# Kernel optimization log

Hardware: AMD Instinct MI355X
Metric: run time of the kernel (lower is better)

Reference implementation:

```python
import jax, jax.numpy as jnp
import numpy as np

DN = ('NCHW', 'OIHW', 'NCHW')

def conv(x, w, b, stride=1, pad=0):
    y = jax.lax.conv_general_dilated(x, w, (stride, stride), ((pad, pad), (pad, pad)), dimension_numbers=DN)
    return y + b[None, :, None, None]

def maxpool(x, k, s):
    return jax.lax.reduce_window(x, -jnp.inf, jax.lax.max, (1, 1, k, k), (1, 1, s, s), 'VALID')

def bilinear_resize(x, oh, ow):
    # torch F.interpolate(mode='bilinear', align_corners=False)
    H, W = x.shape[2], x.shape[3]
    def grid(n_in, n_out):
        c = (jnp.arange(n_out, dtype=x.dtype) + 0.5) * (n_in / n_out) - 0.5
        c = jnp.clip(c, 0.0, n_in - 1)
        lo = jnp.floor(c).astype(jnp.int32)
        hi = jnp.minimum(lo + 1, n_in - 1)
        return lo, hi, c - lo
    r0, r1, wr = grid(H, oh)
    c0, c1, wc = grid(W, ow)
    top = x[:, :, r0, :] * (1 - wr)[None, None, :, None] + x[:, :, r1, :] * wr[None, None, :, None]
    return top[:, :, :, c0] * (1 - wc) + top[:, :, :, c1] * wc

def setup_inputs():
    key = jax.random.key(0)
    ks = jax.random.split(key, 18)
    s = 0.02
    d = {}
    d['x'] = jax.random.normal(ks[0], (16, 3, 448, 448), jnp.float32)
    d['w1'] = jax.random.normal(ks[1], (64, 3, 7, 7), jnp.float32) * s
    d['b1'] = jax.random.normal(ks[2], (64,), jnp.float32) * s
    d['w3'] = jax.random.normal(ks[3], (192, 64, 3, 3), jnp.float32) * s
    d['b3'] = jax.random.normal(ks[4], (192,), jnp.float32) * s
    d['w4'] = jax.random.normal(ks[5], (256, 192, 3, 3), jnp.float32) * s
    d['b4'] = jax.random.normal(ks[6], (256,), jnp.float32) * s
    d['w7'] = jax.random.normal(ks[7], (512, 256, 2, 2), jnp.float32) * s
    d['b7'] = jax.random.normal(ks[8], (512,), jnp.float32) * s
    d['w8'] = jax.random.normal(ks[9], (1024, 512, 2, 2), jnp.float32) * s
    d['b8'] = jax.random.normal(ks[10], (1024,), jnp.float32) * s
    d['wu'] = jax.random.normal(ks[11], (1024, 1024, 2, 2), jnp.float32) * s
    d['bu'] = jax.random.normal(ks[12], (1024,), jnp.float32) * s
    d['lc_w'] = jax.random.normal(ks[13], (1024, 256, 7, 7, 3, 3), jnp.float32) * s
    d['lc_b'] = jax.random.normal(ks[14], (256, 7, 7), jnp.float32) * s
    d['fc_w'] = jax.random.normal(ks[15], (4949, 12544), jnp.float32) * s  # S*S*(C+B*5)=7*7*101
    d['fc_b'] = jax.random.normal(ks[16], (4949,), jnp.float32) * s
    return d

def reference(x, w1, b1, w3, b3, w4, b4, w7, b7, w8, b8, wu, bu, lc_w, lc_b, fc_w, fc_b):
    x = conv(x, w1, b1, 2, 3)        # [B,64,224,224]
    x = maxpool(x, 2, 2)             # 112
    x = conv(x, w3, b3, 1, 1)        # [B,192,112,112]
    x = maxpool(x, 2, 2)             # 56
    x = conv(x, w4, b4)              # [B,256,54,54]
    x = maxpool(x, 2, 2)             # 27
    # CombinedNet backbone not defined in source listing: identity (256->256)
    x = conv(x, w7, b7)              # [B,512,26,26]
    x = maxpool(x, 2, 2)             # 13
    x = conv(x, w8, b8)              # [B,1024,12,12]
    x = conv(x, wu, bu)              # 11 (ultblock applied twice, shared weights)
    x = conv(x, wu, bu)              # 10
    x = maxpool(x, 5, 4)             # [B,1024,2,2]
    x = x[:, :, :14, :14]
    x = bilinear_resize(x, 7, 7)     # [B,1024,7,7]
    # LocallyConnected2d(1024,256,7,7,k=3,s=1,p=1) without materializing the unfold*weight product
    B = x.shape[0]
    xp = jnp.pad(x, ((0, 0), (0, 0), (1, 1), (1, 1)))
    patches = jnp.stack([xp[:, :, i:i + 7, j:j + 7] for i in range(3) for j in range(3)], axis=2)
    patches = patches.reshape(B, 1024, 3, 3, 7, 7)  # [B,C,kh,kw,H,W]
    y = jnp.einsum('bcijhw,cohwij->bohw', patches, lc_w) + lc_b[None]
    y = jnp.where(y > 0, y, 0.1 * y)  # LeakyReLU(0.1)
    # Dropout(p=0.5) is identity at inference; Linear
    y = y.reshape(B, -1) @ fc_w.T + fc_b  # [B,4949]
    return y.reshape(B, 7, 7, 101)
```

## Files before the change

### kernel.cpp

```cpp
#include <hip/hip_runtime.h>

#define UNR _Pragma("unroll")

typedef __attribute__((ext_vector_type(8))) short short8v;
typedef __attribute__((ext_vector_type(4))) float f32x4;

__device__ __forceinline__ ushort f2bf(float f) {
    union { float f; unsigned u; } x; x.f = f;
    unsigned r = (x.u + 0x7fffu + ((x.u >> 16) & 1u)) >> 16;
    return (ushort)r;
}
__device__ __forceinline__ float bf2f(ushort u) {
    union { unsigned u; float f; } x; x.u = ((unsigned)u) << 16;
    return x.f;
}

__device__ __forceinline__ void gll16(const ushort* gp, ushort* lp) {
    __builtin_amdgcn_global_load_lds(
        (const __attribute__((address_space(1))) unsigned int*)(const void*)gp,
        (__attribute__((address_space(3))) unsigned int*)(void*)lp, 16, 0, 0);
}

template<int Wp,int Hp,int OW,int OH,int WpN,int HpN,int PADN,int CN,int WAVES>
__global__ __launch_bounds__(WAVES*64)
void convc1(const ushort* __restrict__ Xp, const ushort* __restrict__ Wb,
            const float* __restrict__ bias, ushort* __restrict__ Yp)
{
    constexpr int CIN = 4, STRIDE = 2, NSTEP = 7;
    constexpr int POW = OW/2, POH = OH/2;
    constexpr int NTOT = 16*POW*POH*4;

    const int lane = (int)threadIdx.x & 63;
    const int wave = (int)threadIdx.x >> 6;
    const int n0   = (blockIdx.y*WAVES + wave) * 64;
    const int lm   = lane & 15;
    const int lk   = lane >> 4;

    int ns[4];
    unsigned boff[4];
    UNR for (int nf=0; nf<4; ++nf) {
        int n = n0 + nf*16 + lm;
        if (n > NTOT-1) n = NTOT-1;
        ns[nf] = n;
        int q = n & 3, pp = n >> 2;
        int px = pp % POW; int t = pp / POW;
        int py = t % POH;  int b = t / POH;
        int oy = 2*py + (q>>1), ox = 2*px + (q&1);
        boff[nf] = ((unsigned)(b*Hp + oy*STRIDE)*Wp + (unsigned)(ox*STRIDE))*CIN
                 + 8u*lk;
    }

    f32x4 acc[4][4];
    UNR for (int i=0;i<4;++i) UNR for (int j=0;j<4;++j) acc[i][j] = f32x4{0.f,0.f,0.f,0.f};

    auto ldfr = [&](int s, short8v (&a)[4], short8v (&bf)[4]) {
        const unsigned xoff = (unsigned)(s*Wp*CIN);
        UNR for (int mf=0; mf<4; ++mf)
            a[mf] = *(const short8v*)(Wb + (unsigned)((s*4 + mf)<<9) + (unsigned)lane*8);
        UNR for (int nf=0; nf<4; ++nf)
            bf[nf] = *(const short8v*)(Xp + boff[nf] + xoff);
    };
    auto dm = [&](short8v (&a)[4], short8v (&bf)[4]) {
        UNR for (int mf=0; mf<4; ++mf)
            UNR for (int nf=0; nf<4; ++nf)
                acc[mf][nf] = __builtin_amdgcn_mfma_f32_16x16x32_bf16(
                                  a[mf], bf[nf], acc[mf][nf], 0, 0, 0);
    };

    short8v aA[4], bA[4], aB[4], bB[4];
    ldfr(0, aA, bA);
    for (int sb = 0; sb < NSTEP; sb += 2) {
        if (sb+1 < NSTEP) ldfr(sb+1, aB, bB);
        dm(aA, bA);
        if (sb+2 < NSTEP) ldfr(sb+2, aA, bA);
        if (sb+1 < NSTEP) dm(aB, bB);
    }

    UNR for (int mf=0; mf<4; ++mf) {
        const int co = mf*16 + 4*lk;
        f32x4 bi = *(const f32x4*)(bias + co);
        UNR for (int nf=0; nf<4; ++nf) {
            f32x4 v = acc[mf][nf];
            UNR for (int r=0;r<4;++r) {
                float t2 = v[r] + bi[r];
                t2 = fmaxf(t2, __shfl_xor(t2 = t2, 1, 64));
                t2 = fmaxf(t2, __shfl_xor(t2, 2, 64));
                v[r] = t2;
            }
            if ((lane & 3) == 0 && (n0 + nf*16 + lm) < NTOT) {
                int pp = ns[nf] >> 2;
                int px = pp % POW; int t2 = pp / POW;
                int py = t2 % POH; int b = t2 / POH;
                unsigned off = ((unsigned)(b*HpN + py + PADN)*WpN
                                + (unsigned)(px + PADN))*CN + co;
                ushort4 s; s.x=f2bf(v[0]); s.y=f2bf(v[1]); s.z=f2bf(v[2]); s.w=f2bf(v[3]);
                *(ushort4*)(Yp + off) = s;
            }
        }
    }
}

template<int CIN,int K,int STRIDE,int Wp,int Hp,int OW,int OH,int COUT,
         bool POOL,int WpN,int HpN,int PADN,int CN,int MT,int NT,int SPLITS>
__global__ __launch_bounds__(256)
void convt(const ushort* __restrict__ Xp, const ushort* __restrict__ Wb,
           const float* __restrict__ bias, ushort* __restrict__ Yp,
           float* __restrict__ part)
{
    static_assert(MT*NT == 4, "4 waves");
    constexpr int POW = OW/2, POH = OH/2;
    constexpr int NTOT = POOL ? 16*POW*POH*4 : 16*OW*OH;
    constexpr int NCH = CIN/32, NSTEP = K*K*NCH;
    constexpr int SPS = NSTEP/SPLITS;
    constexpr int CA = MT*4, CPW = MT + NT;

    const int t    = (int)threadIdx.x;
    const int lane = t & 63;
    const int w    = t >> 6;
    const int mr   = w / NT, nc = w % NT;
    const int cy0  = blockIdx.x * MT;
    const int n0b  = blockIdx.y * (NT*64);
    const int nw0  = n0b + nc*64;
    const int lm   = lane & 15, lk = lane >> 4;
    const int s0   = blockIdx.z * SPS, sE = s0 + SPS;

    __shared__ __align__(1024) ushort Ab[2][CA*512];
    __shared__ __align__(1024) ushort Bb[2][NT*4*512];

    auto nmap = [&](int n, int& b, int& oy, int& ox) {
        if (n > NTOT-1) n = NTOT-1;
        if constexpr (POOL) {
            int q = n & 3, pp = n >> 2;
            int px = pp % POW; int tt = pp / POW;
            int py = tt % POH;  b = tt / POH;
            oy = 2*py + (q>>1); ox = 2*px + (q&1);
        } else {
            ox = n % OW; int tt = n / OW; oy = tt % OH; b = tt / OH;
        }
    };

    int ns[4];
    UNR for (int nf=0; nf<4; ++nf) {
        int n = nw0 + nf*16 + lm;
        if (n > NTOT-1) n = NTOT-1;
        ns[nf] = n;
    }

    unsigned bsrc[CPW];
    UNR for (int j=0; j<CPW; ++j) {
        int q = w*CPW + j;
        if (q >= CA) {
            int bq = q - CA;
            int n = n0b + bq*16 + (lane >> 2);
            int b, oy, ox; nmap(n, b, oy, ox);
            bsrc[j] = ((unsigned)(b*Hp + oy*STRIDE)*Wp + (unsigned)(ox*STRIDE))*CIN
                    + (unsigned)(lane & 3)*8u;
        } else bsrc[j] = 0;
    }

    auto xoffs = [&](int s) -> unsigned {
        int c0  = (s % NCH)*32;
        int kxy = s / NCH;
        int kx  = kxy % K, ky = kxy / K;
        return (unsigned)((ky*Wp + kx)*CIN + c0);
    };
    auto stage = [&](int s, int buf) {
        const unsigned xoff = xoffs(s);
        UNR for (int j=0; j<CPW; ++j) {
            int q = w*CPW + j;
            if (q < CA) {
                const ushort* src = Wb
                    + ((size_t)(((cy0 + (q>>2))*NSTEP + s)*4 + (q&3)) << 9)
                    + (unsigned)lane*8;
                gll16(src, &Ab[buf][(unsigned)q*512u + (unsigned)lane*8u]);
            } else {
                gll16(Xp + bsrc[j] + xoff,
                      &Bb[buf][(unsigned)(q-CA)*512u + (unsigned)lane*8u]);
            }
        }
    };

    f32x4 acc[4][4];
    UNR for (int i=0;i<4;++i) UNR for (int j=0;j<4;++j) acc[i][j] = f32x4{0.f,0.f,0.f,0.f};

    stage(s0, 0);
    __syncthreads();
    int buf = 0;
    for (int s = s0; s < sE; ++s) {
        if (s+1 < sE) stage(s+1, buf^1);
        short8v a[4], bf[4];
        UNR for (int mf=0; mf<4; ++mf)
            a[mf] = *(const short8v*)&Ab[buf][(unsigned)((mr*4+mf)*64 + lane)*8u];
        UNR for (int nf=0; nf<4; ++nf)
            bf[nf] = *(const short8v*)&Bb[buf][(unsigned)((nc*64 + nf*16 + lm)*4 + lk)*8u];
        UNR for (int mf=0; mf<4; ++mf)
            UNR for (int nf=0; nf<4; ++nf)
                acc[mf][nf] = __builtin_amdgcn_mfma_f32_16x16x32_bf16(
                                  a[mf], bf[nf], acc[mf][nf], 0, 0, 0);
        __syncthreads();
        buf ^= 1;
    }

    UNR for (int mf=0; mf<4; ++mf) {
        const int co = (cy0 + mr)*64 + mf*16 + 4*lk;
        if constexpr (SPLITS > 1) {
            UNR for (int nf=0; nf<4; ++nf) {
                if ((nw0 + nf*16 + lm) < NTOT)
                    *(f32x4*)(part + ((size_t)blockIdx.z*NTOT + ns[nf])*COUT + co)
                        = acc[mf][nf];
            }
        } else {
            f32x4 bi = *(const f32x4*)(bias + co);
            UNR for (int nf=0; nf<4; ++nf) {
                f32x4 v = acc[mf][nf];
                UNR for (int r=0;r<4;++r) v[r] += bi[r];
                if constexpr (POOL) {
                    UNR for (int r=0;r<4;++r) {
                        float tt = v[r];
                        tt = fmaxf(tt, __shfl_xor(tt, 1, 64));
                        tt = fmaxf(tt, __shfl_xor(tt, 2, 64));
                        v[r] = tt;
                    }
                    if ((lane & 3) == 0 && (nw0 + nf*16 + lm) < NTOT) {
                        int pp = ns[nf] >> 2;
                        int px = pp % POW; int t2 = pp / POW;
                        int py = t2 % POH; int b = t2 / POH;
                        unsigned off = ((unsigned)(b*HpN + py + PADN)*WpN
                                        + (unsigned)(px + PADN))*CN + co;
                        ushort4 s2; s2.x=f2bf(v[0]); s2.y=f2bf(v[1]); s2.z=f2bf(v[2]); s2.w=f2bf(v[3]);
                        *(ushort4*)(Yp + off) = s2;
                    }
                } else {
                    if ((nw0 + nf*16 + lm) < NTOT) {
                        int n = ns[nf];
                        int ox = n % OW; int t2 = n / OW; int oy = t2 % OH; int b = t2 / OH;
                        unsigned off = ((unsigned)(b*HpN + oy)*WpN + (unsigned)ox)*CN + co;
                        ushort4 s2; s2.x=f2bf(v[0]); s2.y=f2bf(v[1]); s2.z=f2bf(v[2]); s2.w=f2bf(v[3]);
                        *(ushort4*)(Yp + off) = s2;
                    }
                }
            }
        }
    }
}

template<int COUT,int OW,int OH,int WpN,int HpN,int CN,int SPLITS>
__global__ void kreduce(const float* __restrict__ part, const float* __restrict__ bias,
                        ushort* __restrict__ Yp) {
    constexpr int NTOT = 16*OW*OH;
    int idx = blockIdx.x*256 + (int)threadIdx.x;
    if (idx >= NTOT*COUT) return;
    int co = idx % COUT; int n = idx / COUT;
    float sum = 0.f;
    UNR for (int ks=0; ks<SPLITS; ++ks)
        sum += part[((size_t)ks*NTOT + n)*COUT + co];
    sum += bias[co];
    int ox = n % OW; int t = n / OW; int oy = t % OH; int b = t / OH;
    Yp[((unsigned)(b*HpN + oy)*WpN + (unsigned)ox)*CN + co] = f2bf(sum);
}

__global__ void x1build(const float* __restrict__ x, ushort* __restrict__ X1) {
    int idx = blockIdx.x*256 + (int)threadIdx.x;
    int xx = idx % 448; int t = idx/448; int y = t % 448; int b = t/448;
    const float* px = x + ((size_t)b*3*448 + y)*448 + xx;
    ushort4 s;
    s.x = f2bf(px[0]); s.y = f2bf(px[200704]); s.z = f2bf(px[401408]); s.w = 0;
    *(ushort4*)(X1 + ((unsigned)(b*456 + y+3)*456 + (unsigned)(xx+3))*4) = s;
}

__global__ void wcvt1(const float* __restrict__ w, ushort* __restrict__ o) {
    int idx = blockIdx.x*256 + (int)threadIdx.x;
    if (idx >= 14336) return;
    int e = idx & 7; int t = idx >> 3;
    int lane = t & 63; t >>= 6;
    int mf = t & 3; int s = t >> 2;
    int co = mf*16 + (lane & 15);
    int cc = (lane >> 4)*8 + e;
    int kx = cc >> 2, ci = cc & 3;
    float v = 0.f;
    if (kx < 7 && ci < 3) v = w[(((size_t)co*3 + ci)*7 + s)*7 + kx];
    o[idx] = f2bf(v);
}

template<int CIN,int K,int COUT>
__global__ void wcvt(const float* __restrict__ w, ushort* __restrict__ o) {
    constexpr int NCH = CIN/32, NSTEP = K*K*NCH;
    int idx = blockIdx.x*256 + (int)threadIdx.x;
    if (idx >= COUT*K*K*CIN) return;
    int e = idx & 7; int t = idx >> 3;
    int lane = t & 63; t >>= 6;
    int mf = t & 3; t >>= 2;
    int s = t % NSTEP; int cy = t / NSTEP;
    int co = cy*64 + mf*16 + (lane & 15);
    int kxy = s / NCH, ch = s % NCH;
    int ci = ch*32 + (lane >> 4)*8 + e;
    int ky = kxy / K, kx = kxy % K;
    o[idx] = f2bf(w[(((size_t)co*CIN + ci)*K + ky)*K + kx]);
}

__global__ void pool54_k(const ushort* __restrict__ in, float* __restrict__ out) {
    int idx = blockIdx.x*256 + (int)threadIdx.x;
    int c = idx & 1023; int t = idx >> 10; int q = t & 3; int b = t >> 2;
    int i = q >> 1, j = q & 1;
    float m = -1e30f;
    UNR for (int r=0;r<5;++r)
        UNR for (int cc=0;cc<5;++cc)
            m = fmaxf(m, bf2f(in[(((unsigned)(b*10 + i*4+r))*10 + (unsigned)(j*4+cc))*1024 + c]));
    out[((size_t)(b*1024 + c))*4 + q] = m;
}

__device__ __forceinline__ void bigrid(int k, int& lo, float& f) {
    float c = ((float)k + 0.5f) * (2.0f/7.0f) - 0.5f;
    c = fminf(fmaxf(c, 0.f), 1.f);
    float fl = floorf(c);
    lo = (int)fl;
    f = c - fl;
}

__global__ void buildPb(const float* __restrict__ pp, ushort* __restrict__ Pb) {
    int idx = blockIdx.x*256 + (int)threadIdx.x;
    int k = idx & 15;
    int c = (idx >> 4) & 1023;
    int r = idx >> 14;
    int b = r & 15; int hw = r >> 4;
    float val = 0.f;
    if (k < 9) {
        int i = k/3, j = k%3;
        int h = hw/7, w2 = hw%7;
        int rr = h + i - 1, cc = w2 + j - 1;
        if (rr>=0 && rr<7 && cc>=0 && cc<7) {
            int rlo; float rf; bigrid(rr, rlo, rf);
            int clo; float cf; bigrid(cc, clo, cf);
            int rhi = min(rlo+1,1), chi = min(clo+1,1);
            const float* qq = pp + ((size_t)(b*1024 + c))*4;
            float v00=qq[rlo*2+clo], v01=qq[rlo*2+chi], v10=qq[rhi*2+clo], v11=qq[rhi*2+chi];
            float top = v00*(1.f-cf) + v01*cf;
            float bot = v10*(1.f-cf) + v11*cf;
            val = top*(1.f-rf) + bot*rf;
        }
    }
    Pb[idx] = f2bf(val);
}

__global__ __launch_bounds__(256)
void lconv_fused(const float* __restrict__ lcw, const ushort* __restrict__ Pb,
                 float* __restrict__ part) {
    const int bid = (int)blockIdx.x;
    const int xcd = bid & 7;
    const int i   = bid >> 3;
    const int hw  = i % 49;
    const int ks  = xcd + 8*(i/49);
    const int t   = (int)threadIdx.x;
    const int lane = t & 63, w = t >> 6;
    const int lm = lane & 15, lk = lane >> 4;
    const int c0 = ks*64;

    __shared__ ushort A[2][8192];

    auto ldreg = [&](int cc, float (&w9)[2][9]) {
        const int cb = c0 + cc*2;
        UNR for (int cl=0; cl<2; ++cl) {
            const float* src = lcw + ((size_t)(cb+cl)*256 + (unsigned)(w*64+lane))*441
                             + hw*9;
            __builtin_memcpy(w9[cl], src, 36);
        }
    };
    auto wrlds = [&](int buf, float (&w9)[2][9]) {
        UNR for (int cl=0; cl<2; ++cl) {
            int rem = cl*256 + w*64 + lane;
            ushort u[16];
            UNR for (int k=0;k<8;++k) u[k]=f2bf(w9[cl][k]);
            u[8]=f2bf(w9[cl][8]);
            UNR for (int k=9;k<16;++k) u[k]=0;
            *(short8v*)&A[buf][(unsigned)rem*8u] = *(short8v*)&u[0];
            *(short8v*)&A[buf][4096u + (unsigned)rem*8u] = *(short8v*)&u[8];
        }
    };

    f32x4 acc[4];
    UNR for (int q=0;q<4;++q) acc[q] = f32x4{0.f,0.f,0.f,0.f};

    const ushort* Bb = Pb + (size_t)(hw*16 + lm)*16384 + ks*1024 + lk*8;
    const int arow = (lk&1)*512 + (lk>>1)*256 + w*64 + lm;

    auto mmac = [&](int buf, int cc) {
        short8v bv = *(const short8v*)(Bb + cc*32);
        UNR for (int mf = 0; mf < 4; ++mf) {
            short8v av = *(const short8v*)&A[buf][(unsigned)(arow + mf*16)*8u];
            acc[mf] = __builtin_amdgcn_mfma_f32_16x16x32_bf16(av, bv, acc[mf], 0,0,0);
        }
    };

    float wA[2][9], wB[2][9];
    ldreg(0, wA);
    wrlds(0, wA);
    ldreg(1, wB);
    for (int cc = 0; cc < 32; cc += 2) {
        mmac(0, cc);
        wrlds(1, wB);
        if (cc+2 < 32) ldreg(cc+2, wA);
        mmac(1, cc+1);
        if (cc+2 < 32) {
            wrlds(0, wA);
            if (cc+3 < 32) ldreg(cc+3, wB);
        }
    }

    UNR for (int mf=0; mf<4; ++mf)
        UNR for (int r=0;r<4;++r) {
            int o = w*64 + mf*16 + 4*lk + r;
            part[(((size_t)ks*49 + hw)*256 + o)*16 + lm] = acc[mf][r];
        }
}

__global__ void lreduce2(const float* __restrict__ part, const float* __restrict__ lcb,
                         float* __restrict__ yact) {
    int idx = blockIdx.x*256 + (int)threadIdx.x;
    int b = idx & 15; int o = (idx >> 4) & 255; int hw = idx >> 12;
    float sum = 0.f;
    UNR for (int ks=0; ks<16; ++ks)
        sum += part[(((size_t)ks*49 + hw)*256 + o)*16 + b];
    sum += lcb[o*49 + hw];
    float v = (sum > 0.f) ? sum : 0.1f*sum;
    yact[b*12544 + o*49 + hw] = v;
}

__global__ __launch_bounds__(256)
void fc_k(const float* __restrict__ act, const float* __restrict__ fw,
          const float* __restrict__ fb, float* __restrict__ out) {
    __shared__ float alds[16][256];
    __shared__ float red[4][4][16];
    const int t = (int)threadIdx.x;
    const int o0 = blockIdx.x*4;
    float acc[4][16];
    UNR for (int oo=0;oo<4;++oo) UNR for (int b=0;b<16;++b) acc[oo][b]=0.f;

    for (int k0=0; k0<12544; k0+=256) {
        __syncthreads();
        UNR for (int b=0;b<16;++b) alds[b][t] = act[b*12544 + k0 + t];
        __syncthreads();
        float wv[4];
        UNR for (int oo=0;oo<4;++oo) {
            int o = o0+oo;
            wv[oo] = (o < 4949) ? fw[(size_t)o*12544 + k0 + t] : 0.f;
        }
        UNR for (int b=0;b<16;++b) {
            float av = alds[b][t];
            UNR for (int oo=0;oo<4;++oo) acc[oo][b] = fmaf(wv[oo], av, acc[oo][b]);
        }
    }
    UNR for (int oo=0;oo<4;++oo)
        UNR for (int b=0;b<16;++b) {
            float v = acc[oo][b];
            UNR for (int off=32; off; off>>=1) v += __shfl_xor(v, off, 64);
            acc[oo][b] = v;
        }
    const int wave = t>>6, lane = t&63;
    if (lane == 0)
        UNR for (int oo=0;oo<4;++oo)
            UNR for (int b=0;b<16;++b) red[wave][oo][b] = acc[oo][b];
    __syncthreads();
    if (t < 64) {
        int oo = t>>4, b = t&15;
        float v = red[0][oo][b]+red[1][oo][b]+red[2][oo][b]+red[3][oo][b];
        int o = o0+oo;
        if (o < 4949) out[b*4949 + o] = v + fb[o];
    }
}

extern "C" void kernel_launch(void* const* d_in, const int* in_sizes, int n_in,
                              void* d_out, int out_size, void* d_ws, size_t ws_size,
                              hipStream_t stream) {
    const float* x   = (const float*)d_in[0];
    const float* w1  = (const float*)d_in[1];
    const float* b1  = (const float*)d_in[2];
    const float* w3  = (const float*)d_in[3];
    const float* b3  = (const float*)d_in[4];
    const float* w4  = (const float*)d_in[5];
    const float* b4  = (const float*)d_in[6];
    const float* w7  = (const float*)d_in[7];
    const float* b7  = (const float*)d_in[8];
    const float* w8  = (const float*)d_in[9];
    const float* b8  = (const float*)d_in[10];
    const float* wu  = (const float*)d_in[11];
    const float* bu  = (const float*)d_in[12];
    const float* lcw = (const float*)d_in[13];
    const float* lcb = (const float*)d_in[14];
    const float* fw  = (const float*)d_in[15];
    const float* fb  = (const float*)d_in[16];
    float* out = (float*)d_out;

    char* base = (char*)d_ws;
    auto alloc = [&](size_t bytes) { char* p = base; base += (bytes + 255) & ~(size_t)255; return p; };
    ushort* X1  = (ushort*)alloc(16u*456*456*4*2);
    ushort* X3  = (ushort*)alloc(16u*114*114*64*2);
    ushort* X4  = (ushort*)alloc(16u*56*56*192*2);
    ushort* X7  = (ushort*)alloc(16u*27*27*256*2);
    ushort* X8  = (ushort*)alloc(16u*13*13*512*2);
    ushort* XU1 = (ushort*)alloc(16u*12*12*1024*2);
    ushort* XU2 = (ushort*)alloc(16u*11*11*1024*2);
    ushort* XU3 = (ushort*)alloc(16u*10*10*1024*2);
    ushort* W1b = (ushort*)alloc(64u*224*2);
    ushort* W3b = (ushort*)alloc(192u*576*2);
    ushort* W4b = (ushort*)alloc(256u*1728*2);
    ushort* W7b = (ushort*)alloc(512u*1024*2);
    ushort* W8b = (ushort*)alloc(1024u*2048*2);
    ushort* WUb = (ushort*)alloc(1024u*4096*2);
    float*  pp  = (float*)alloc(16u*1024*4*4);
    ushort* Pb  = (ushort*)alloc((size_t)49*16*16384*2);
    float*  part = (float*)alloc((size_t)16*49*256*16*4);
    float*  partK = (float*)alloc((size_t)4*2304*1024*4);
    float*  yact = (float*)X7;

    hipMemsetAsync(X1, 0, 16u*456*456*4*2, stream);
    hipMemsetAsync(X3, 0, 16u*114*114*64*2, stream);
    x1build<<<12544, 256, 0, stream>>>(x, X1);
    wcvt1<<<56, 256, 0, stream>>>(w1, W1b);
    wcvt<64,3,192><<<432, 256, 0, stream>>>(w3, W3b);
    wcvt<192,3,256><<<1728, 256, 0, stream>>>(w4, W4b);
    wcvt<256,2,512><<<2048, 256, 0, stream>>>(w7, W7b);
    wcvt<512,2,1024><<<8192, 256, 0, stream>>>(w8, W8b);
    wcvt<1024,2,1024><<<16384, 256, 0, stream>>>(wu, WUb);

    convc1<456,456,224,224,114,114,1,64, 4>
        <<<dim3(1,3136), 256, 0, stream>>>(X1, W1b, b1, X3);
    convt<64,3,1,114,114,112,112,192, true,56,56,0,192, 1,4,1>
        <<<dim3(3,784,1), 256, 0, stream>>>(X3, W3b, b3, X4, nullptr);
    convt<192,3,1,56,56,54,54,256, true,27,27,0,256, 2,2,1>
        <<<dim3(2,365,1), 256, 0, stream>>>(X4, W4b, b4, X7, nullptr);
    convt<256,2,1,27,27,26,26,512, true,13,13,0,512, 2,2,1>
        <<<dim3(4,85,1), 256, 0, stream>>>(X7, W7b, b7, X8, nullptr);
    convt<512,2,1,13,13,12,12,1024, false,12,12,0,1024, 2,2,4>
        <<<dim3(8,18,4), 256, 0, stream>>>(X8, W8b, nullptr, nullptr, partK);
    kreduce<1024,12,12,12,12,1024,4><<<9216, 256, 0, stream>>>(partK, b8, XU1);
    convt<1024,2,1,12,12,11,11,1024, false,11,11,0,1024, 2,2,4>
        <<<dim3(8,16,4), 256, 0, stream>>>(XU1, WUb, nullptr, nullptr, partK);
    kreduce<1024,11,11,11,11,1024,4><<<7744, 256, 0, stream>>>(partK, bu, XU2);
    convt<1024,2,1,11,11,10,10,1024, false,10,10,0,1024, 2,2,4>
        <<<dim3(8,13,4), 256, 0, stream>>>(XU2, WUb, nullptr, nullptr, partK);
    kreduce<1024,10,10,10,10,1024,4><<<6400, 256, 0, stream>>>(partK, bu, XU3);

    pool54_k<<<256, 256, 0, stream>>>(XU3, pp);
    buildPb<<<50176, 256, 0, stream>>>(pp, Pb);
    lconv_fused<<<784, 256, 0, stream>>>(lcw, Pb, part);
    lreduce2<<<784, 256, 0, stream>>>(part, lcb, yact);
    fc_k<<<1238, 256, 0, stream>>>(yact, fw, fb, out);
}
```

Baseline: 806.7 us.

## Triple-buffer convt LDS staging with explicit vmcnt waits and MFMA priority

Replaces the double-buffered load/compute loop in the tiled conv kernel with a three-stage ring buffer. Each iteration issues async global-to-LDS loads two steps ahead and waits only on the older loads with explicit vmcnt counts and a raw s_barrier, so memory latency can be hidden behind more MFMA work. It also raises wave priority around the MFMA block. In exchange it uses 50% more shared memory, which may reduce occupancy, and requires at least three steps per split. The hand-written vmcnt values must match the per-wave load count exactly to stay correct.

```diff
diff --git a/kernel.cpp b/kernel.cpp
--- a/kernel.cpp
+++ b/kernel.cpp
@@ -19,6 +19,19 @@
     __builtin_amdgcn_global_load_lds(
         (const __attribute__((address_space(1))) unsigned int*)(const void*)gp,
         (__attribute__((address_space(3))) unsigned int*)(void*)lp, 16, 0, 0);
+}
+
+template<int N> __device__ __forceinline__ void waitvm() {
+    if constexpr (N == 0)       asm volatile("s_waitcnt vmcnt(0)" ::: "memory");
+    else if constexpr (N == 4)  asm volatile("s_waitcnt vmcnt(4)" ::: "memory");
+    else if constexpr (N == 5)  asm volatile("s_waitcnt vmcnt(5)" ::: "memory");
+    else if constexpr (N == 8)  asm volatile("s_waitcnt vmcnt(8)" ::: "memory");
+    else if constexpr (N == 10) asm volatile("s_waitcnt vmcnt(10)" ::: "memory");
+    __builtin_amdgcn_sched_barrier(0);
+}
+__device__ __forceinline__ void blockbar() {
+    __builtin_amdgcn_s_barrier();
+    __builtin_amdgcn_sched_barrier(0);
 }
 
 template<int Wp,int Hp,int OW,int OH,int WpN,int HpN,int PADN,int CN,int WAVES>
@@ -83,7 +96,7 @@
             f32x4 v = acc[mf][nf];
             UNR for (int r=0;r<4;++r) {
                 float t2 = v[r] + bi[r];
-                t2 = fmaxf(t2, __shfl_xor(t2 = t2, 1, 64));
+                t2 = fmaxf(t2, __shfl_xor(t2, 1, 64));
                 t2 = fmaxf(t2, __shfl_xor(t2, 2, 64));
                 v[r] = t2;
             }
@@ -112,7 +125,8 @@
     constexpr int NTOT = POOL ? 16*POW*POH*4 : 16*OW*OH;
     constexpr int NCH = CIN/32, NSTEP = K*K*NCH;
     constexpr int SPS = NSTEP/SPLITS;
-    constexpr int CA = MT*4, CPW = MT + NT;
+    static_assert(SPS >= 3, "pipeline depth");
+    constexpr int CA = MT*4, CB = NT*4, CPW = MT + NT;
 
     const int t    = (int)threadIdx.x;
     const int lane = t & 63;
@@ -124,8 +138,8 @@
     const int lm   = lane & 15, lk = lane >> 4;
     const int s0   = blockIdx.z * SPS, sE = s0 + SPS;
 
-    __shared__ __align__(1024) ushort Ab[2][CA*512];
-    __shared__ __align__(1024) ushort Bb[2][NT*4*512];
+    __shared__ __align__(1024) ushort Ab[3][CA*512];
+    __shared__ __align__(1024) ushort Bb[3][CB*512];
 
     auto nmap = [&](int n, int& b, int& oy, int& ox) {
         if (n > NTOT-1) n = NTOT-1;
@@ -183,23 +197,36 @@
     f32x4 acc[4][4];
     UNR for (int i=0;i<4;++i) UNR for (int j=0;j<4;++j) acc[i][j] = f32x4{0.f,0.f,0.f,0.f};
 
-    stage(s0, 0);
-    __syncthreads();
-    int buf = 0;
-    for (int s = s0; s < sE; ++s) {
-        if (s+1 < sE) stage(s+1, buf^1);
+    auto compute = [&](int buf) {
         short8v a[4], bf[4];
         UNR for (int mf=0; mf<4; ++mf)
             a[mf] = *(const short8v*)&Ab[buf][(unsigned)((mr*4+mf)*64 + lane)*8u];
         UNR for (int nf=0; nf<4; ++nf)
             bf[nf] = *(const short8v*)&Bb[buf][(unsigned)((nc*64 + nf*16 + lm)*4 + lk)*8u];
+        __builtin_amdgcn_s_setprio(1);
         UNR for (int mf=0; mf<4; ++mf)
             UNR for (int nf=0; nf<4; ++nf)
                 acc[mf][nf] = __builtin_amdgcn_mfma_f32_16x16x32_bf16(
                                   a[mf], bf[nf], acc[mf][nf], 0, 0, 0);
-        __syncthreads();
-        buf ^= 1;
-    }
+        __builtin_amdgcn_s_setprio(0);
+    };
+
+    stage(s0, 0);
+    stage(s0+1, 1);
+    int s = s0;
+    for (; s < sE-2; ++s) {
+        waitvm<CPW>();
+        blockbar();
+        stage(s+2, (s+2-s0)%3);
+        compute((s-s0)%3);
+    }
+    waitvm<CPW>();
+    blockbar();
+    compute((s-s0)%3);
+    ++s;
+    waitvm<0>();
+    blockbar();
+    compute((s-s0)%3);
 
     UNR for (int mf=0; mf<4; ++mf) {
         const int co = (cy0 + mr)*64 + mf*16 + 4*lk;
```

Measured after the change: 809.4 us. No clear change (+0.3%).
